# Kernel optimization log

Measured on AMD Instinct MI355X. Metric: run time of the kernel, lower is better.

The kernel has to match this reference:

```python
import jax, jax.numpy as jnp
import numpy as np

NUM_BINS = 32
LAMBDA_W2 = 0.1
SMOOTHING = 1e-3
LABEL_SMOOTHING = 0.05


def setup_inputs() -> dict:
    key = jax.random.key(0)
    k1, k2, k3 = jax.random.split(key, 3)
    B, H, W = 64, 512, 512
    return {
        "changes_obs": jax.random.normal(k1, (B, H, W), dtype=jnp.float32),
        "changes_pred": jax.random.normal(k2, (B, H, W), dtype=jnp.float32),
        "mask": jax.random.randint(k3, (B, H, W), 0, 2).astype(bool),
        "bin_edges": jnp.linspace(-3.0, 3.0, NUM_BINS + 1, dtype=jnp.float32),
    }


def compute_histogram(changes, bin_edges, mask):
    # changes, mask: [B, H, W]; bin_edges: [num_bins+1]
    B = changes.shape[0]
    num_bins = bin_edges.shape[0] - 1
    x = changes.reshape(B, -1)                      # [B, N]
    m = mask.reshape(B, -1)                         # [B, N]
    # bucketize: bin i is [e_i, e_{i+1}), last bin closed on the right
    idx = jnp.searchsorted(bin_edges, x, side='right') - 1
    idx = jnp.clip(idx, 0, num_bins - 1)            # x == last edge -> last bin
    valid = m & (x >= bin_edges[0]) & (x <= bin_edges[-1])
    flat = (jnp.arange(B)[:, None] * num_bins + idx).reshape(-1)
    counts = jax.ops.segment_sum(
        valid.reshape(-1).astype(jnp.float32), flat, num_segments=B * num_bins
    ).reshape(B, num_bins)
    # torch: a sample with zero masked pixels gets counts of all ones
    n_masked = m.sum(axis=1)
    counts = jnp.where((n_masked == 0)[:, None], 1.0, counts)
    total = jnp.maximum(counts.sum(axis=1, keepdims=True), 1.0)
    proportions = counts / total
    return counts, proportions


def reference(changes_obs, changes_pred, mask, bin_edges):
    num_bins = bin_edges.shape[0] - 1
    _, p_obs = compute_histogram(changes_obs, bin_edges, mask)
    _, p_pred = compute_histogram(changes_pred, bin_edges, mask)
    p_pred = (1.0 - LABEL_SMOOTHING) * p_pred + LABEL_SMOOTHING / num_bins
    # class-balanced weights from observed proportions
    avg = p_obs.mean(axis=0)
    w = 1.0 / (avg + SMOOTHING)
    w = w * num_bins / w.sum()
    ce_loss = (-p_obs * jnp.log(p_pred + 1e-8) * w[None, :]).sum(axis=1).mean()
    # Wasserstein-2 on CDFs with midpoint-spacing bin widths
    mid = 0.5 * (bin_edges[:-1] + bin_edges[1:])
    bw = mid[1:] - mid[:-1]
    bw = jnp.concatenate([bw, bw[-1:]])
    cdf_obs = jnp.cumsum(p_obs, axis=1)
    cdf_pred = jnp.cumsum(p_pred, axis=1)
    w2_loss = (((cdf_obs - cdf_pred) ** 2) * bw[None, :]).sum(axis=1).mean()
    total_loss = (ce_loss + LAMBDA_W2 * w2_loss) / num_bins
    return total_loss, ce_loss, w2_loss, p_obs, p_pred
```

## Files before the change

### kernel.cpp

```cpp
#include <hip/hip_runtime.h>
#include <stdint.h>

#define NBINS 32
#define NBATCH 64
#define NPB (512 * 512)
#define BPB 32
#define TPB 256
#define EPB (NPB / BPB)
#define ITERS (EPB / (TPB * 4))

#define WS_PRED 2048
#define WS_NM   4096
#define WS_FLAG 4160
#define WS_WORDS 4161

__global__ void detect_mask_kernel(const uint32_t* __restrict__ mw,
                                   uint32_t* __restrict__ flag) {
  uint32_t v = mw[threadIdx.x];
  if (__any(v > 1u) && threadIdx.x == 0) *flag = 1u;
}

__device__ __forceinline__ int bin_of(float x) {
  float t = __builtin_fmaf(x, 5.333333492279053f, 16.0f);
  int i = (int)t;
  float fi = (float)i;
  float elo = __builtin_fmaf(fi, 0.1875f, -3.0f);
  float ehi = elo + 0.1875f;
  i += (x >= ehi) ? 1 : 0;
  i -= (x < elo) ? 1 : 0;
  return i;
}

__device__ __forceinline__ void count_one(int i, uint32_t h[8]) {
  const uint32_t inc = 1u << ((i & 3) << 3);
  const int hi = i >> 2;
#pragma unroll
  for (int r = 0; r < 8; ++r) h[r] += (hi == r) ? inc : 0u;
}

__global__ __launch_bounds__(TPB) void hist_kernel(
    const float* __restrict__ obs, const float* __restrict__ pred,
    const void* __restrict__ mask, uint32_t* __restrict__ ws) {
  __shared__ uint32_t red[4][32];

  const int tid = threadIdx.x;
  const uint32_t is_u8 = ws[WS_FLAG];
  const int b = blockIdx.x / BPB;
  const int chunk = blockIdx.x % BPB;
  const size_t base_f4 = (((size_t)b * NPB) + ((size_t)chunk * EPB)) >> 2;

  const float4* __restrict__ o4 = (const float4*)obs;
  const float4* __restrict__ p4 = (const float4*)pred;
  const uint32_t* __restrict__ mwp = (const uint32_t*)mask;
  const int4* __restrict__ mip = (const int4*)mask;

  uint32_t c[8] = {0, 0, 0, 0, 0, 0, 0, 0};
  uint32_t d[8] = {0, 0, 0, 0, 0, 0, 0, 0};
  uint32_t nm_pack = 0;
  uint32_t nm_cnt = 0;

#pragma unroll
  for (int it = 0; it < ITERS; ++it) {
    const size_t idx = base_f4 + (size_t)(it * TPB + tid);
    const float4 xo = o4[idx];
    const float4 xp = p4[idx];

    bool m0, m1, m2, m3;
    if (is_u8) {
      const uint32_t w = mwp[idx];
      nm_pack += w;
      m0 = (w & 0x000000ffu) != 0u;
      m1 = (w & 0x0000ff00u) != 0u;
      m2 = (w & 0x00ff0000u) != 0u;
      m3 = (w & 0xff000000u) != 0u;
    } else {
      const int4 mv = mip[idx];
      m0 = mv.x != 0; m1 = mv.y != 0; m2 = mv.z != 0; m3 = mv.w != 0;
      nm_cnt += (m0 ? 1u : 0u) + (m1 ? 1u : 0u) + (m2 ? 1u : 0u) + (m3 ? 1u : 0u);
    }

    const float a0 = m0 ? xo.x : 1e2f, b0 = m0 ? xp.x : 1e2f;
    const float a1 = m1 ? xo.y : 1e2f, b1 = m1 ? xp.y : 1e2f;
    const float a2 = m2 ? xo.z : 1e2f, b2 = m2 ? xp.z : 1e2f;
    const float a3 = m3 ? xo.w : 1e2f, b3 = m3 ? xp.w : 1e2f;

    count_one(bin_of(a0), c); count_one(bin_of(b0), d);
    count_one(bin_of(a1), c); count_one(bin_of(b1), d);
    count_one(bin_of(a2), c); count_one(bin_of(b2), d);
    count_one(bin_of(a3), c); count_one(bin_of(b3), d);
  }

  uint32_t nm = is_u8 ? ((nm_pack & 0xffu) + ((nm_pack >> 8) & 0xffu) +
                         ((nm_pack >> 16) & 0xffu) + (nm_pack >> 24))
                      : nm_cnt;
#pragma unroll
  for (int off = 32; off >= 1; off >>= 1) nm += __shfl_down(nm, off);
  if ((tid & 63) == 0) atomicAdd(&ws[WS_NM + b], nm);

#pragma unroll
  for (int m = 1; m <= 2; m <<= 1) {
#pragma unroll
    for (int r = 0; r < 8; ++r) {
      c[r] += __shfl_xor(c[r], m);
      d[r] += __shfl_xor(d[r], m);
    }
  }
  uint32_t cl[8], ch[8], dl[8], dh[8];
#pragma unroll
  for (int r = 0; r < 8; ++r) {
    cl[r] = c[r] & 0x00FF00FFu; ch[r] = (c[r] >> 8) & 0x00FF00FFu;
    dl[r] = d[r] & 0x00FF00FFu; dh[r] = (d[r] >> 8) & 0x00FF00FFu;
  }
#pragma unroll
  for (int m = 4; m <= 32; m <<= 1) {
#pragma unroll
    for (int r = 0; r < 8; ++r) {
      cl[r] += __shfl_xor(cl[r], m); ch[r] += __shfl_xor(ch[r], m);
      dl[r] += __shfl_xor(dl[r], m); dh[r] += __shfl_xor(dh[r], m);
    }
  }

  const int w = tid >> 6;
  if ((tid & 63) == 0) {
#pragma unroll
    for (int r = 0; r < 8; ++r) {
      red[w][r] = cl[r];
      red[w][8 + r] = ch[r];
      red[w][16 + r] = dl[r];
      red[w][24 + r] = dh[r];
    }
  }
  __syncthreads();

  if (tid < 2 * NBINS) {
    const int arr = tid >> 5;
    const int bin = tid & 31;
    const int slot = arr * 16 + (bin >> 2) + ((bin & 1) ? 8 : 0);
    const int shift = (bin & 2) ? 16 : 0;
    uint32_t s = 0;
#pragma unroll
    for (int wv = 0; wv < 4; ++wv) s += (red[wv][slot] >> shift) & 0xFFFFu;
    if (s) atomicAdd(&ws[(arr ? WS_PRED : 0) + b * NBINS + bin], s);
  }
}

__global__ __launch_bounds__(64) void finalize_kernel(
    const uint32_t* __restrict__ ws, const float* __restrict__ edges,
    float* __restrict__ out) {
  __shared__ float pobs[NBATCH][NBINS + 1];
  __shared__ float ppred[NBATCH][NBINS + 1];
  __shared__ float w_sh[NBINS];
  __shared__ float bw_sh[NBINS];
  __shared__ float w_scale;

  const int t = threadIdx.x;

  const uint32_t* co = ws + t * NBINS;
  const uint32_t* cp = ws + WS_PRED + t * NBINS;
  const uint32_t nmask = ws[WS_NM + t];

  float sum_o = 0.0f, sum_p = 0.0f;
#pragma unroll
  for (int j = 0; j < NBINS; ++j) {
    float vo = (nmask == 0u) ? 1.0f : (float)co[j];
    float vp = (nmask == 0u) ? 1.0f : (float)cp[j];
    pobs[t][j] = vo;  sum_o += vo;
    ppred[t][j] = vp; sum_p += vp;
  }
  const float inv_to = 1.0f / fmaxf(sum_o, 1.0f);
  const float inv_tp = 1.0f / fmaxf(sum_p, 1.0f);
#pragma unroll
  for (int j = 0; j < NBINS; ++j) {
    pobs[t][j] *= inv_to;
    ppred[t][j] = 0.95f * (ppred[t][j] * inv_tp) + 0.05f / (float)NBINS;
  }
  __syncthreads();

  if (t < NBINS) {
    float s = 0.0f;
#pragma unroll
    for (int b = 0; b < NBATCH; ++b) s += pobs[b][t];
    const float avg = s / (float)NBATCH;
    w_sh[t] = 1.0f / (avg + 1e-3f);
    const int j2 = (t < NBINS - 1) ? t : (NBINS - 2);
    const float mA = 0.5f * (edges[j2] + edges[j2 + 1]);
    const float mB = 0.5f * (edges[j2 + 1] + edges[j2 + 2]);
    bw_sh[t] = mB - mA;
  }
  __syncthreads();
  if (t == 0) {
    float sw = 0.0f;
#pragma unroll
    for (int j = 0; j < NBINS; ++j) sw += w_sh[j];
    w_scale = (float)NBINS / sw;
  }
  __syncthreads();

  float ce = 0.0f, w2 = 0.0f, cdf_o = 0.0f, cdf_p = 0.0f;
#pragma unroll
  for (int j = 0; j < NBINS; ++j) {
    const float po = pobs[t][j];
    const float pp = ppred[t][j];
    ce += -po * logf(pp + 1e-8f) * (w_sh[j] * w_scale);
    cdf_o += po;
    cdf_p += pp;
    const float dd = cdf_o - cdf_p;
    w2 += dd * dd * bw_sh[j];
  }

  float ce_r = ce, w2_r = w2;
#pragma unroll
  for (int off = 32; off >= 1; off >>= 1) {
    ce_r += __shfl_down(ce_r, off);
    w2_r += __shfl_down(w2_r, off);
  }
  if (t == 0) {
    const float ce_m = ce_r / (float)NBATCH;
    const float w2_m = w2_r / (float)NBATCH;
    out[0] = (ce_m + 0.1f * w2_m) / (float)NBINS;
    out[1] = ce_m;
    out[2] = w2_m;
  }

#pragma unroll
  for (int j = 0; j < NBINS; ++j) {
    out[3 + t * NBINS + j] = pobs[t][j];
    out[3 + NBATCH * NBINS + t * NBINS + j] = ppred[t][j];
  }
}

extern "C" void kernel_launch(void* const* d_in, const int* in_sizes, int n_in,
                              void* d_out, int out_size, void* d_ws,
                              size_t ws_size, hipStream_t stream) {
  const float* obs = (const float*)d_in[0];
  const float* pred = (const float*)d_in[1];
  const void* mask = d_in[2];
  const float* edges = (const float*)d_in[3];
  float* out = (float*)d_out;
  uint32_t* ws = (uint32_t*)d_ws;

  hipMemsetAsync(d_ws, 0, WS_WORDS * sizeof(uint32_t), stream);
  detect_mask_kernel<<<1, 64, 0, stream>>>((const uint32_t*)mask,
                                           ws + WS_FLAG);
  hist_kernel<<<NBATCH * BPB, TPB, 0, stream>>>(obs, pred, mask, ws);
  finalize_kernel<<<1, 64, 0, stream>>>(ws, edges, out);
}
```

Baseline: 246.7 us.

## Interleave block access pattern and software-prefetch next iteration loads in histogram

Each block now reads an interleaved set of float4 slots strided by BPB*TPB across its batch, instead of one contiguous chunk. The loop also double-buffers, issuing the next iteration's obs, pred and mask loads before binning the current ones. Launch bounds now request 8 waves per SIMD to raise occupancy. The goal is to hide memory latency in this bandwidth-bound kernel, at the cost of more live registers and a changed DRAM access locality per block.

Measured after the change: 263.3 us. 6.8% more time.

```diff
diff --git a/kernel.cpp b/kernel.cpp
--- a/kernel.cpp
+++ b/kernel.cpp
@@ -6,8 +6,7 @@
 #define NPB (512 * 512)
 #define BPB 32
 #define TPB 256
-#define EPB (NPB / BPB)
-#define ITERS (EPB / (TPB * 4))
+#define ITERS 8
 
 #define WS_PRED 2048
 #define WS_NM   4096
@@ -38,7 +37,7 @@
   for (int r = 0; r < 8; ++r) h[r] += (hi == r) ? inc : 0u;
 }
 
-__global__ __launch_bounds__(TPB) void hist_kernel(
+__global__ __launch_bounds__(TPB, 8) void hist_kernel(
     const float* __restrict__ obs, const float* __restrict__ pred,
     const void* __restrict__ mask, uint32_t* __restrict__ ws) {
   __shared__ uint32_t red[4][32];
@@ -47,7 +46,8 @@
   const uint32_t is_u8 = ws[WS_FLAG];
   const int b = blockIdx.x / BPB;
   const int chunk = blockIdx.x % BPB;
-  const size_t base_f4 = (((size_t)b * NPB) + ((size_t)chunk * EPB)) >> 2;
+
+  const size_t bbase = (size_t)b * (NPB / 4) + (size_t)chunk * TPB + tid;
 
   const float4* __restrict__ o4 = (const float4*)obs;
   const float4* __restrict__ p4 = (const float4*)pred;
@@ -59,23 +59,36 @@
   uint32_t nm_pack = 0;
   uint32_t nm_cnt = 0;
 
+  float4 xo, xp;
+  uint32_t mw_c = 0;
+  int4 mi_c = {0, 0, 0, 0};
+  {
+    xo = o4[bbase];
+    xp = p4[bbase];
+    if (is_u8) mw_c = mwp[bbase]; else mi_c = mip[bbase];
+  }
+
 #pragma unroll
   for (int it = 0; it < ITERS; ++it) {
-    const size_t idx = base_f4 + (size_t)(it * TPB + tid);
-    const float4 xo = o4[idx];
-    const float4 xp = p4[idx];
+    float4 nxo = xo, nxp = xp;
+    uint32_t nmw = mw_c;
+    int4 nmi = mi_c;
+    if (it + 1 < ITERS) {
+      const size_t ni = bbase + (size_t)(it + 1) * (BPB * TPB);
+      nxo = o4[ni];
+      nxp = p4[ni];
+      if (is_u8) nmw = mwp[ni]; else nmi = mip[ni];
+    }
 
     bool m0, m1, m2, m3;
     if (is_u8) {
-      const uint32_t w = mwp[idx];
-      nm_pack += w;
-      m0 = (w & 0x000000ffu) != 0u;
-      m1 = (w & 0x0000ff00u) != 0u;
-      m2 = (w & 0x00ff0000u) != 0u;
-      m3 = (w & 0xff000000u) != 0u;
+      nm_pack += mw_c;
+      m0 = (mw_c & 0x000000ffu) != 0u;
+      m1 = (mw_c & 0x0000ff00u) != 0u;
+      m2 = (mw_c & 0x00ff0000u) != 0u;
+      m3 = (mw_c & 0xff000000u) != 0u;
     } else {
-      const int4 mv = mip[idx];
-      m0 = mv.x != 0; m1 = mv.y != 0; m2 = mv.z != 0; m3 = mv.w != 0;
+      m0 = mi_c.x != 0; m1 = mi_c.y != 0; m2 = mi_c.z != 0; m3 = mi_c.w != 0;
       nm_cnt += (m0 ? 1u : 0u) + (m1 ? 1u : 0u) + (m2 ? 1u : 0u) + (m3 ? 1u : 0u);
     }
 
@@ -88,6 +101,8 @@
     count_one(bin_of(a1), c); count_one(bin_of(b1), d);
     count_one(bin_of(a2), c); count_one(bin_of(b2), d);
     count_one(bin_of(a3), c); count_one(bin_of(b3), d);
+
+    xo = nxo; xp = nxp; mw_c = nmw; mi_c = nmi;
   }
 
   uint32_t nm = is_u8 ? ((nm_pack & 0xffu) + ((nm_pack >> 8) & 0xffu) +
```
